# Optimization experiments

Hardware: AMD Instinct MI355X
Metric: run time of the kernel (lower is better)

The kernel has to match this reference:

```python
import jax, jax.numpy as jnp
import numpy as np

N = 50000
E = 600000
D = 128


def gcn_conv(x, row, col, w, W, b):
    """PyG GCNConv: add self-loops (weight 1), symmetric deg^-1/2 normalization,
    linear transform, edge-weighted scatter-add aggregation, then bias."""
    n = x.shape[0]
    loop = jnp.arange(n)
    r = jnp.concatenate([row, loop])            # source nodes, [E+N]
    c = jnp.concatenate([col, loop])            # target nodes, [E+N]
    ww = jnp.concatenate([w, jnp.ones((n,), x.dtype)])
    deg = jax.ops.segment_sum(ww, c, num_segments=n)          # weighted in-degree
    dinv = jnp.where(deg > 0, jax.lax.rsqrt(deg), jnp.zeros_like(deg))
    norm = dinv[r] * ww * dinv[c]               # [E+N]
    xl = x @ W                                  # [n, D_out]
    msg = norm[:, None] * xl[r]                 # gather + scale, [E+N, D_out]
    out = jax.ops.segment_sum(msg, c, num_segments=n)
    return out + b


def setup_inputs() -> dict:
    key = jax.random.key(0)
    ks = jax.random.split(key, 12)
    x = jax.random.normal(ks[0], (N, D), dtype=jnp.float32)
    edge_index = jax.random.randint(ks[1], (2, E), 0, N, dtype=jnp.int64)
    edge_weights = jax.random.uniform(ks[2], (E,), dtype=jnp.float32)
    s = 1.0 / np.sqrt(D)
    W1 = jax.random.uniform(ks[3], (D, D), jnp.float32, -s, s)
    b1 = jnp.zeros((D,), jnp.float32)
    W2 = jax.random.uniform(ks[4], (D, D), jnp.float32, -s, s)
    b2 = jnp.zeros((D,), jnp.float32)
    W3 = jax.random.uniform(ks[5], (D, D), jnp.float32, -s, s)
    b3 = jnp.zeros((D,), jnp.float32)
    prelu_w = jnp.array(0.25, jnp.float32)
    return {"x": x, "edge_index": edge_index, "edge_weights": edge_weights,
            "W1": W1, "b1": b1, "W2": W2, "b2": b2, "W3": W3, "b3": b3,
            "prelu_w": prelu_w}


def reference(x, edge_index, edge_weights, W1, b1, W2, b2, W3, b3, prelu_w):
    row, col = edge_index[0], edge_index[1]
    # layer 1: GCNConv -> (dropout: eval, identity) -> ELU
    h = gcn_conv(x, row, col, edge_weights, W1, b1)
    h = jax.nn.elu(h)
    # layer 2: GCNConv -> GELU (torch default = exact erf)
    h = gcn_conv(h, row, col, edge_weights, W2, b2)
    h = jax.nn.gelu(h, approximate=False)
    # layer 3: GCNConv -> PReLU (learnable scalar slope)
    h = gcn_conv(h, row, col, edge_weights, W3, b3)
    h = jnp.where(h >= 0, h, prelu_w * h)
    return h
```

## Files before the change

### kernel.cpp

```cpp
#include <hip/hip_runtime.h>
#include <hip/hip_fp16.h>
#include <math.h>
#include <string.h>

constexpr int D = 128;

struct __align__(16) H8 { __half2 h[4]; };
struct __align__(8)  H4 { __half2 a, b; };

typedef _Float16 half8  __attribute__((ext_vector_type(8)));
typedef float   floatx4 __attribute__((ext_vector_type(4)));
typedef int     i32x4   __attribute__((ext_vector_type(4)));

template <typename T>
__device__ __forceinline__ T ld_nt(const T* p) {
  if constexpr (sizeof(T) == 16) {
    i32x4 v = __builtin_nontemporal_load((const i32x4*)p);
    T r; memcpy(&r, &v, 16); return r;
  } else {
    int v = __builtin_nontemporal_load((const int*)p);
    T r; memcpy(&r, &v, 4); return r;
  }
}
__device__ __forceinline__ void st_nt16(void* p, float4 v) {
  i32x4 t; memcpy(&t, &v, 16);
  __builtin_nontemporal_store(t, (i32x4*)p);
}


__device__ __forceinline__ int detect64(const int* __restrict__ ei) {
  int z = 0;
#pragma unroll
  for (int i = 0; i < 8; ++i) z |= ei[2 * i + 1];
  return (z == 0) ? 1 : 0;
}

__device__ __forceinline__ void load_edge(const int* __restrict__ ei, int e, int nE,
                                          int m64, int n, int& r, int& c) {
  if (m64) { r = ei[2 * (size_t)e]; c = ei[2 * ((size_t)nE + e)]; }
  else     { r = ei[(size_t)e];     c = ei[(size_t)nE + e]; }
  r = min(max(r, 0), n - 1);
  c = min(max(c, 0), n - 1);
}

__global__ void k_init(const float* __restrict__ W1, const float* __restrict__ W2,
                       const float* __restrict__ W3, __half* __restrict__ Wt,
                       int* __restrict__ cnt, int n) {
  __shared__ float s[128][129];
  int tid = threadIdx.x;
  if (blockIdx.x >= 3) {
    int i = (blockIdx.x - 3) * 256 + tid;
    if (i < n) cnt[i] = 0;
    return;
  }
  const float* W = blockIdx.x == 0 ? W1 : (blockIdx.x == 1 ? W2 : W3);
  __half* o = Wt + (size_t)blockIdx.x * D * D;
#pragma unroll
  for (int i = 0; i < 16; ++i) {
    int flat = i * 1024 + tid * 4;
    int k = flat >> 7;
    int nn = flat & 127;
    float4 v = *(const float4*)(W + (size_t)k * D + nn);
    s[k][nn] = v.x; s[k][nn + 1] = v.y; s[k][nn + 2] = v.z; s[k][nn + 3] = v.w;
  }
  __syncthreads();
#pragma unroll
  for (int i = 0; i < 8; ++i) {
    int flat = i * 256 + tid;
    int nn = flat >> 4;
    int k0 = (flat & 15) * 8;
    H8 hv;
#pragma unroll
    for (int t = 0; t < 4; ++t)
      hv.h[t] = __floats2half2_rn(s[k0 + 2 * t][nn], s[k0 + 2 * t + 1][nn]);
    *(H8*)(o + (size_t)nn * D + k0) = hv;
  }
}

__global__ void k_pos(const int* __restrict__ ei, int* __restrict__ cnt,
                      unsigned int* __restrict__ rcp, int* __restrict__ pos,
                      int nE, int n) {
  int e = blockIdx.x * blockDim.x + threadIdx.x;
  if (e >= nE) return;
  int m64 = detect64(ei);
  int r, c;
  load_edge(ei, e, nE, m64, n, r, c);
  rcp[e] = ((unsigned int)r << 16) | (unsigned int)c;
  pos[e] = atomicAdd(&cnt[c], 1);
}

__global__ void k_scan1(const int* __restrict__ cnt, int* __restrict__ offs,
                        int* __restrict__ bsum, int n) {
  __shared__ int s[256];
  int t = threadIdx.x;
  int i = blockIdx.x * 256 + t;
  int v = (i < n) ? cnt[i] : 0;
  s[t] = v;
  __syncthreads();
  for (int off = 1; off < 256; off <<= 1) {
    int x = 0;
    if (t >= off) x = s[t - off];
    __syncthreads();
    if (t >= off) s[t] += x;
    __syncthreads();
  }
  if (i < n) offs[i] = s[t] - v;
  if (t == 255) bsum[blockIdx.x] = s[255];
}

__global__ void k_scan2(const int* __restrict__ bsum, int* __restrict__ boff, int nb) {
  __shared__ int s[256];
  int t = threadIdx.x;
  int v = (t < nb) ? bsum[t] : 0;
  s[t] = v;
  __syncthreads();
  for (int off = 1; off < 256; off <<= 1) {
    int x = 0;
    if (t >= off) x = s[t - off];
    __syncthreads();
    if (t >= off) s[t] += x;
    __syncthreads();
  }
  if (t < nb) boff[t] = s[t] - v;
}

__global__ void k_scan3(int* __restrict__ offs, const int* __restrict__ boff, int n, int nE) {
  int i = blockIdx.x * 256 + threadIdx.x;
  if (i < n) offs[i] += boff[blockIdx.x];
  if (i == 0) offs[n] = nE;
}

__global__ void k_fill(const unsigned int* __restrict__ rcp, const int* __restrict__ pos,
                       const float* __restrict__ w, const int* __restrict__ offs,
                       int2* __restrict__ ecf, int nE) {
  int e = blockIdx.x * blockDim.x + threadIdx.x;
  if (e >= nE) return;
  unsigned int p = rcp[e];
  int idx = offs[p & 0xffffu] + pos[e];
  ecf[idx] = make_int2((int)(p >> 16), __float_as_int(w[e]));
}

__global__ void k_degdinv(const int2* __restrict__ ecf, const int* __restrict__ offs,
                          float* __restrict__ dinv, int n) {
  int i = blockIdx.x * blockDim.x + threadIdx.x;
  if (i >= n) return;
  float s = 1.0f;
  int e1 = offs[i + 1];
  for (int e = offs[i]; e < e1; ++e) s += __int_as_float(ecf[e].y);
  dinv[i] = rsqrtf(s);
}

__global__ void k_coef(const int2* __restrict__ ecf, const float* __restrict__ dinv,
                       unsigned int* __restrict__ ecf2, int nE) {
  int e = blockIdx.x * blockDim.x + threadIdx.x;
  if (e >= nE) return;
  int2 p = ecf[e];
  float c = dinv[p.x] * __int_as_float(p.y);
  ecf2[e] = ((unsigned int)p.x << 16) |
            (unsigned int)__half_as_ushort(__float2half_rn(c));
}

template <int ACT>
__device__ __forceinline__ float act_f(float x) {
  if (ACT == 1) return x > 0.f ? x : expm1f(x);
  if (ACT == 2) return 0.5f * x * (1.0f + erff(x * 0.70710678118654752440f));
  return x;
}

template <int ACT, typename AT>
__global__ __launch_bounds__(256) void k_gemm(const AT* __restrict__ A,
                                              const __half* __restrict__ Wt,
                                              __half* __restrict__ Y, int n) {
  const int wave = threadIdx.x >> 6;
  const int lane = threadIdx.x & 63;
  const int np = lane & 15;
  const int quad = lane >> 4;
  const int node = blockIdx.x * 64 + wave * 16 + np;
  const int nc = min(node, n - 1);

  half8 b[4];
#pragma unroll
  for (int s = 0; s < 4; ++s) {
    if constexpr (sizeof(AT) == 4) {
      const float* ap = (const float*)A + (size_t)nc * D + s * 32 + quad * 8;
      float4 v0 = ld_nt((const float4*)ap);
      float4 v1 = ld_nt((const float4*)(ap + 4));
      b[s][0] = (_Float16)act_f<ACT>(v0.x); b[s][1] = (_Float16)act_f<ACT>(v0.y);
      b[s][2] = (_Float16)act_f<ACT>(v0.z); b[s][3] = (_Float16)act_f<ACT>(v0.w);
      b[s][4] = (_Float16)act_f<ACT>(v1.x); b[s][5] = (_Float16)act_f<ACT>(v1.y);
      b[s][6] = (_Float16)act_f<ACT>(v1.z); b[s][7] = (_Float16)act_f<ACT>(v1.w);
    } else {
      half8 raw = *(const half8*)((const __half*)A + ((size_t)s * n + nc) * 32 + quad * 8);
#pragma unroll
      for (int t = 0; t < 8; ++t)
        b[s][t] = (_Float16)act_f<ACT>((float)raw[t]);
    }
  }

  floatx4 acc[8];
#pragma unroll
  for (int mt = 0; mt < 8; ++mt) acc[mt] = (floatx4){0.f, 0.f, 0.f, 0.f};

#pragma unroll
  for (int mt = 0; mt < 8; ++mt) {
#pragma unroll
    for (int s = 0; s < 4; ++s) {
      half8 a = *(const half8*)(Wt + (size_t)(mt * 16 + np) * D + s * 32 + quad * 8);
      acc[mt] = __builtin_amdgcn_mfma_f32_16x16x32_f16(a, b[s], acc[mt], 0, 0, 0);
    }
  }

  if (node < n) {
#pragma unroll
    for (int mt = 0; mt < 8; ++mt) {
      H4 hv;
      hv.a = __floats2half2_rn(acc[mt][0], acc[mt][1]);
      hv.b = __floats2half2_rn(acc[mt][2], acc[mt][3]);
      int f0 = mt * 16 + quad * 4;
      *(H4*)(Y + ((size_t)(f0 >> 5) * n + node) * 32 + (f0 & 31)) = hv;
    }
  }
}

__device__ __forceinline__ void fmacc8(float* acc, float c, const H8& y) {
  float2 f;
  f = __half22float2(y.h[0]); acc[0] += c * f.x; acc[1] += c * f.y;
  f = __half22float2(y.h[1]); acc[2] += c * f.x; acc[3] += c * f.y;
  f = __half22float2(y.h[2]); acc[4] += c * f.x; acc[5] += c * f.y;
  f = __half22float2(y.h[3]); acc[6] += c * f.x; acc[7] += c * f.y;
}

__device__ __forceinline__ float cdecode(unsigned int u) {
  return __half2float(__ushort_as_half((unsigned short)(u & 0xffffu)));
}

template <int PRELU, typename OutT>
__global__ __launch_bounds__(256) void k_agg(const __half* __restrict__ Y,
                                             const int* __restrict__ offs,
                                             const unsigned int* __restrict__ ecf2,
                                             const float* __restrict__ dinv,
                                             const float* __restrict__ bias,
                                             const float* __restrict__ pw,
                                             OutT* __restrict__ OUT, int n) {
  const int chunk = blockIdx.x & 3;
  const int t = threadIdx.x;
  const int node = (blockIdx.x >> 2) * 32 + (t >> 3);
  const int sub = (t >> 2) & 1;
  const int j = t & 3;
  if (node >= n) return;
  const __half* Yc = Y + (size_t)chunk * n * 32;
  float dc = dinv[node];
  float acc[8] = {0.f, 0.f, 0.f, 0.f, 0.f, 0.f, 0.f, 0.f};
  if (sub == 0) {
    H8 ys = *(const H8*)(Yc + (size_t)node * 32 + j * 8);
    fmacc8(acc, dc, ys);
  }
  int e0 = offs[node], e1 = offs[node + 1];
  int e = e0 + sub;
  for (; e + 6 < e1; e += 8) {
    unsigned int u0 = ld_nt(&ecf2[e]),     u1 = ld_nt(&ecf2[e + 2]);
    unsigned int u2 = ld_nt(&ecf2[e + 4]), u3 = ld_nt(&ecf2[e + 6]);
    H8 y0 = *(const H8*)(Yc + (size_t)(u0 >> 16) * 32 + j * 8);
    H8 y1 = *(const H8*)(Yc + (size_t)(u1 >> 16) * 32 + j * 8);
    H8 y2 = *(const H8*)(Yc + (size_t)(u2 >> 16) * 32 + j * 8);
    H8 y3 = *(const H8*)(Yc + (size_t)(u3 >> 16) * 32 + j * 8);
    fmacc8(acc, cdecode(u0), y0);
    fmacc8(acc, cdecode(u1), y1);
    fmacc8(acc, cdecode(u2), y2);
    fmacc8(acc, cdecode(u3), y3);
  }
  for (; e + 2 < e1; e += 4) {
    unsigned int u0 = ld_nt(&ecf2[e]), u1 = ld_nt(&ecf2[e + 2]);
    H8 y0 = *(const H8*)(Yc + (size_t)(u0 >> 16) * 32 + j * 8);
    H8 y1 = *(const H8*)(Yc + (size_t)(u1 >> 16) * 32 + j * 8);
    fmacc8(acc, cdecode(u0), y0);
    fmacc8(acc, cdecode(u1), y1);
  }
  for (; e < e1; e += 2) {
    unsigned int u = ld_nt(&ecf2[e]);
    H8 y = *(const H8*)(Yc + (size_t)(u >> 16) * 32 + j * 8);
    fmacc8(acc, cdecode(u), y);
  }
#pragma unroll
  for (int i = 0; i < 8; ++i) acc[i] += __shfl_xor(acc[i], 4, 64);
  float4 b4 = *(const float4*)(bias + chunk * 32 + j * 8 + sub * 4);
  float o[4];
  o[0] = dc * acc[sub * 4 + 0] + b4.x;
  o[1] = dc * acc[sub * 4 + 1] + b4.y;
  o[2] = dc * acc[sub * 4 + 2] + b4.z;
  o[3] = dc * acc[sub * 4 + 3] + b4.w;
  if (PRELU) {
    float wv = *pw;
#pragma unroll
    for (int i = 0; i < 4; ++i) o[i] = o[i] >= 0.f ? o[i] : wv * o[i];
  }
  if constexpr (sizeof(OutT) == 4) {
    st_nt16((float*)OUT + (size_t)node * D + chunk * 32 + j * 8 + sub * 4,
            make_float4(o[0], o[1], o[2], o[3]));
  } else {
    H4 hv;
    hv.a = __floats2half2_rn(o[0], o[1]);
    hv.b = __floats2half2_rn(o[2], o[3]);
    *(H4*)((__half*)OUT + ((size_t)chunk * n + node) * 32 + j * 8 + sub * 4) = hv;
  }
}

extern "C" void kernel_launch(void* const* d_in, const int* in_sizes, int n_in,
                              void* d_out, int out_size, void* d_ws, size_t ws_size,
                              hipStream_t stream) {
  const float* x  = (const float*)d_in[0];
  const int*   ei = (const int*)d_in[1];
  const float* w  = (const float*)d_in[2];
  const float* W1 = (const float*)d_in[3];
  const float* b1 = (const float*)d_in[4];
  const float* W2 = (const float*)d_in[5];
  const float* b2 = (const float*)d_in[6];
  const float* W3 = (const float*)d_in[7];
  const float* b3 = (const float*)d_in[8];
  const float* pw = (const float*)d_in[9];
  const int N = in_sizes[0] / D;
  const int E = in_sizes[2];
  float* out = (float*)d_out;

  char* wsb = (char*)d_ws;
  size_t off = 0;
  auto alloc = [&](size_t bytes) {
    void* p = wsb + off;
    off = (off + bytes + 255) & ~(size_t)255;
    return p;
  };
  float*        dinv = (float*)alloc((size_t)N * 4);
  int*          cnt  = (int*)alloc((size_t)N * 4);
  int*          offs = (int*)alloc((size_t)(N + 1) * 4);
  int*          bsum = (int*)alloc(256 * 4);
  int*          boff = (int*)alloc(256 * 4);
  int2*         ecf  = (int2*)alloc((size_t)E * 8);
  unsigned int* ecf2 = (unsigned int*)alloc((size_t)E * 4);
  __half*       Wt   = (__half*)alloc((size_t)3 * D * D * 2);
  __half*       Y    = (__half*)alloc((size_t)N * D * 2);
  __half*       h    = (__half*)alloc((size_t)N * D * 2);
  unsigned int* rcp  = (unsigned int*)Y;
  int*          pos  = (int*)((char*)Y + (size_t)E * 4);

  const int nb = (N + 255) / 256;
  const int eb = (E + 255) / 256;

  hipLaunchKernelGGL(k_init,    dim3(3 + nb), dim3(256), 0, stream, W1, W2, W3, Wt, cnt, N);
  hipLaunchKernelGGL(k_pos,     dim3(eb), dim3(256), 0, stream, ei, cnt, rcp, pos, E, N);
  hipLaunchKernelGGL(k_scan1,   dim3(nb), dim3(256), 0, stream, cnt, offs, bsum, N);
  hipLaunchKernelGGL(k_scan2,   dim3(1),  dim3(256), 0, stream, bsum, boff, nb);
  hipLaunchKernelGGL(k_scan3,   dim3(nb), dim3(256), 0, stream, offs, boff, N, E);
  hipLaunchKernelGGL(k_fill,    dim3(eb), dim3(256), 0, stream, rcp, pos, w, offs, ecf, E);
  hipLaunchKernelGGL(k_degdinv, dim3(nb), dim3(256), 0, stream, ecf, offs, dinv, N);
  hipLaunchKernelGGL(k_coef,    dim3(eb), dim3(256), 0, stream, ecf, dinv, ecf2, E);

  const int gb = (N + 63) / 64;
  const int ab = 4 * ((N + 31) / 32);

  hipLaunchKernelGGL((k_gemm<0, float>),  dim3(gb), dim3(256), 0, stream, x, Wt,             Y, N);
  hipLaunchKernelGGL((k_agg<0, __half>),  dim3(ab), dim3(256), 0, stream, Y, offs, ecf2, dinv, b1, pw, h, N);
  hipLaunchKernelGGL((k_gemm<1, __half>), dim3(gb), dim3(256), 0, stream, h, Wt + D * D,     Y, N);
  hipLaunchKernelGGL((k_agg<0, __half>),  dim3(ab), dim3(256), 0, stream, Y, offs, ecf2, dinv, b2, pw, h, N);
  hipLaunchKernelGGL((k_gemm<2, __half>), dim3(gb), dim3(256), 0, stream, h, Wt + 2 * D * D, Y, N);
  hipLaunchKernelGGL((k_agg<1, float>),   dim3(ab), dim3(256), 0, stream, Y, offs, ecf2, dinv, b3, pw, out, N);
}
```

Measured before the change: 328.7 us.

## Fold source dinv into GEMM output, drop coef pass, single-block scan, wider agg split

The source-side normalisation dinv[r] moves into the GEMM epilogue, so Z = dinv*xW and the edge coefficient becomes just the raw weight stored as fp16. This removes the k_coef kernel and the 8-byte ecf intermediate. The three-kernel scan becomes one 1024-thread single-block scan built on wave shuffles. The aggregation kernel now uses 16 threads per node-chunk (4 edge lanes instead of 2) with an extra shuffle reduction, and drops nontemporal loads on the edge list. The trade-off is that the serial single-block scan may be slower, and storing edge weights in fp16 before the degree sum costs some precision.

New measurement: 344.2 us. 1.05x slower.

```diff
diff --git a/kernel.cpp b/kernel.cpp
--- a/kernel.cpp
+++ b/kernel.cpp
@@ -14,17 +14,12 @@
 
 template <typename T>
 __device__ __forceinline__ T ld_nt(const T* p) {
-  if constexpr (sizeof(T) == 16) {
-    i32x4 v = __builtin_nontemporal_load((const i32x4*)p);
-    T r; memcpy(&r, &v, 16); return r;
-  } else {
-    int v = __builtin_nontemporal_load((const int*)p);
-    T r; memcpy(&r, &v, 4); return r;
-  }
-}
-__device__ __forceinline__ void st_nt16(void* p, float4 v) {
-  i32x4 t; memcpy(&t, &v, 16);
-  __builtin_nontemporal_store(t, (i32x4*)p);
+  i32x4 v = __builtin_nontemporal_load((const i32x4*)p);
+  T r; memcpy(&r, &v, 16); return r;
+}
+__device__ __forceinline__ void st_nt8(void* p, float2 v) {
+  long long t; memcpy(&t, &v, 8);
+  __builtin_nontemporal_store(t, (long long*)p);
 }
 
 
@@ -89,75 +84,63 @@
   pos[e] = atomicAdd(&cnt[c], 1);
 }
 
-__global__ void k_scan1(const int* __restrict__ cnt, int* __restrict__ offs,
-                        int* __restrict__ bsum, int n) {
-  __shared__ int s[256];
-  int t = threadIdx.x;
-  int i = blockIdx.x * 256 + t;
-  int v = (i < n) ? cnt[i] : 0;
-  s[t] = v;
-  __syncthreads();
-  for (int off = 1; off < 256; off <<= 1) {
-    int x = 0;
-    if (t >= off) x = s[t - off];
+__global__ __launch_bounds__(1024) void k_scan(const int* __restrict__ cnt,
+                                               int* __restrict__ offs, int n, int nE) {
+  __shared__ int wsx[16];
+  __shared__ int tot;
+  const int t = threadIdx.x;
+  const int lane = t & 63, wid = t >> 6;
+  int carry = 0;
+  for (int base = 0; base < n; base += 1024) {
+    int i = base + t;
+    int v = (i < n) ? cnt[i] : 0;
+    int s = v;
+#pragma unroll
+    for (int d = 1; d < 64; d <<= 1) {
+      int x = __shfl_up(s, d, 64);
+      if (lane >= d) s += x;
+    }
+    if (lane == 63) wsx[wid] = s;
     __syncthreads();
-    if (t >= off) s[t] += x;
+    if (t < 16) {
+      int ws = wsx[t];
+      int ss = ws;
+#pragma unroll
+      for (int d = 1; d < 16; d <<= 1) {
+        int x = __shfl_up(ss, d, 16);
+        if (t >= d) ss += x;
+      }
+      wsx[t] = ss - ws;
+      if (t == 15) tot = ss;
+    }
     __syncthreads();
-  }
-  if (i < n) offs[i] = s[t] - v;
-  if (t == 255) bsum[blockIdx.x] = s[255];
-}
-
-__global__ void k_scan2(const int* __restrict__ bsum, int* __restrict__ boff, int nb) {
-  __shared__ int s[256];
-  int t = threadIdx.x;
-  int v = (t < nb) ? bsum[t] : 0;
-  s[t] = v;
-  __syncthreads();
-  for (int off = 1; off < 256; off <<= 1) {
-    int x = 0;
-    if (t >= off) x = s[t - off];
+    if (i < n) offs[i] = carry + wsx[wid] + (s - v);
+    carry += tot;
     __syncthreads();
-    if (t >= off) s[t] += x;
-    __syncthreads();
-  }
-  if (t < nb) boff[t] = s[t] - v;
-}
-
-__global__ void k_scan3(int* __restrict__ offs, const int* __restrict__ boff, int n, int nE) {
-  int i = blockIdx.x * 256 + threadIdx.x;
-  if (i < n) offs[i] += boff[blockIdx.x];
-  if (i == 0) offs[n] = nE;
+  }
+  if (t == 0) offs[n] = nE;
 }
 
 __global__ void k_fill(const unsigned int* __restrict__ rcp, const int* __restrict__ pos,
                        const float* __restrict__ w, const int* __restrict__ offs,
-                       int2* __restrict__ ecf, int nE) {
+                       unsigned int* __restrict__ ecf2, int nE) {
   int e = blockIdx.x * blockDim.x + threadIdx.x;
   if (e >= nE) return;
   unsigned int p = rcp[e];
   int idx = offs[p & 0xffffu] + pos[e];
-  ecf[idx] = make_int2((int)(p >> 16), __float_as_int(w[e]));
-}
-
-__global__ void k_degdinv(const int2* __restrict__ ecf, const int* __restrict__ offs,
+  ecf2[idx] = (p & 0xffff0000u) |
+              (unsigned int)__half_as_ushort(__float2half_rn(w[e]));
+}
+
+__global__ void k_degdinv(const unsigned int* __restrict__ ecf2, const int* __restrict__ offs,
                           float* __restrict__ dinv, int n) {
   int i = blockIdx.x * blockDim.x + threadIdx.x;
   if (i >= n) return;
   float s = 1.0f;
   int e1 = offs[i + 1];
-  for (int e = offs[i]; e < e1; ++e) s += __int_as_float(ecf[e].y);
+  for (int e = offs[i]; e < e1; ++e)
+    s += __half2float(__ushort_as_half((unsigned short)(ecf2[e] & 0xffffu)));
   dinv[i] = rsqrtf(s);
-}
-
-__global__ void k_coef(const int2* __restrict__ ecf, const float* __restrict__ dinv,
-                       unsigned int* __restrict__ ecf2, int nE) {
-  int e = blockIdx.x * blockDim.x + threadIdx.x;
-  if (e >= nE) return;
-  int2 p = ecf[e];
-  float c = dinv[p.x] * __int_as_float(p.y);
-  ecf2[e] = ((unsigned int)p.x << 16) |
-            (unsigned int)__half_as_ushort(__float2half_rn(c));
 }
 
 template <int ACT>
@@ -170,7 +153,8 @@
 template <int ACT, typename AT>
 __global__ __launch_bounds__(256) void k_gemm(const AT* __restrict__ A,
                                               const __half* __restrict__ Wt,
-                                              __half* __restrict__ Y, int n) {
+                                              const float* __restrict__ dinv,
+                                              __half* __restrict__ Z, int n) {
   const int wave = threadIdx.x >> 6;
   const int lane = threadIdx.x & 63;
   const int np = lane & 15;
@@ -211,13 +195,14 @@
   }
 
   if (node < n) {
+    float dv = dinv[node];
 #pragma unroll
     for (int mt = 0; mt < 8; ++mt) {
       H4 hv;
-      hv.a = __floats2half2_rn(acc[mt][0], acc[mt][1]);
-      hv.b = __floats2half2_rn(acc[mt][2], acc[mt][3]);
+      hv.a = __floats2half2_rn(dv * acc[mt][0], dv * acc[mt][1]);
+      hv.b = __floats2half2_rn(dv * acc[mt][2], dv * acc[mt][3]);
       int f0 = mt * 16 + quad * 4;
-      *(H4*)(Y + ((size_t)(f0 >> 5) * n + node) * 32 + (f0 & 31)) = hv;
+      *(H4*)(Z + ((size_t)(f0 >> 5) * n + node) * 32 + (f0 & 31)) = hv;
     }
   }
 }
@@ -235,7 +220,7 @@
 }
 
 template <int PRELU, typename OutT>
-__global__ __launch_bounds__(256) void k_agg(const __half* __restrict__ Y,
+__global__ __launch_bounds__(256) void k_agg(const __half* __restrict__ Z,
                                              const int* __restrict__ offs,
                                              const unsigned int* __restrict__ ecf2,
                                              const float* __restrict__ dinv,
@@ -244,64 +229,62 @@
                                              OutT* __restrict__ OUT, int n) {
   const int chunk = blockIdx.x & 3;
   const int t = threadIdx.x;
-  const int node = (blockIdx.x >> 2) * 32 + (t >> 3);
-  const int sub = (t >> 2) & 1;
+  const int node = (blockIdx.x >> 2) * 16 + (t >> 4);
+  const int sub = (t >> 2) & 3;
   const int j = t & 3;
   if (node >= n) return;
-  const __half* Yc = Y + (size_t)chunk * n * 32;
-  float dc = dinv[node];
+  const __half* Zc = Z + (size_t)chunk * n * 32;
   float acc[8] = {0.f, 0.f, 0.f, 0.f, 0.f, 0.f, 0.f, 0.f};
   if (sub == 0) {
-    H8 ys = *(const H8*)(Yc + (size_t)node * 32 + j * 8);
-    fmacc8(acc, dc, ys);
+    H8 zs = *(const H8*)(Zc + (size_t)node * 32 + j * 8);
+    fmacc8(acc, 1.0f, zs);
   }
   int e0 = offs[node], e1 = offs[node + 1];
   int e = e0 + sub;
-  for (; e + 6 < e1; e += 8) {
-    unsigned int u0 = ld_nt(&ecf2[e]),     u1 = ld_nt(&ecf2[e + 2]);
-    unsigned int u2 = ld_nt(&ecf2[e + 4]), u3 = ld_nt(&ecf2[e + 6]);
-    H8 y0 = *(const H8*)(Yc + (size_t)(u0 >> 16) * 32 + j * 8);
-    H8 y1 = *(const H8*)(Yc + (size_t)(u1 >> 16) * 32 + j * 8);
-    H8 y2 = *(const H8*)(Yc + (size_t)(u2 >> 16) * 32 + j * 8);
-    H8 y3 = *(const H8*)(Yc + (size_t)(u3 >> 16) * 32 + j * 8);
-    fmacc8(acc, cdecode(u0), y0);
-    fmacc8(acc, cdecode(u1), y1);
-    fmacc8(acc, cdecode(u2), y2);
-    fmacc8(acc, cdecode(u3), y3);
-  }
-  for (; e + 2 < e1; e += 4) {
-    unsigned int u0 = ld_nt(&ecf2[e]), u1 = ld_nt(&ecf2[e + 2]);
-    H8 y0 = *(const H8*)(Yc + (size_t)(u0 >> 16) * 32 + j * 8);
-    H8 y1 = *(const H8*)(Yc + (size_t)(u1 >> 16) * 32 + j * 8);
-    fmacc8(acc, cdecode(u0), y0);
-    fmacc8(acc, cdecode(u1), y1);
-  }
-  for (; e < e1; e += 2) {
-    unsigned int u = ld_nt(&ecf2[e]);
-    H8 y = *(const H8*)(Yc + (size_t)(u >> 16) * 32 + j * 8);
-    fmacc8(acc, cdecode(u), y);
-  }
-#pragma unroll
-  for (int i = 0; i < 8; ++i) acc[i] += __shfl_xor(acc[i], 4, 64);
-  float4 b4 = *(const float4*)(bias + chunk * 32 + j * 8 + sub * 4);
-  float o[4];
-  o[0] = dc * acc[sub * 4 + 0] + b4.x;
-  o[1] = dc * acc[sub * 4 + 1] + b4.y;
-  o[2] = dc * acc[sub * 4 + 2] + b4.z;
-  o[3] = dc * acc[sub * 4 + 3] + b4.w;
+  for (; e + 12 < e1; e += 16) {
+    unsigned int u0 = ecf2[e],     u1 = ecf2[e + 4];
+    unsigned int u2 = ecf2[e + 8], u3 = ecf2[e + 12];
+    H8 z0 = *(const H8*)(Zc + (size_t)(u0 >> 16) * 32 + j * 8);
+    H8 z1 = *(const H8*)(Zc + (size_t)(u1 >> 16) * 32 + j * 8);
+    H8 z2 = *(const H8*)(Zc + (size_t)(u2 >> 16) * 32 + j * 8);
+    H8 z3 = *(const H8*)(Zc + (size_t)(u3 >> 16) * 32 + j * 8);
+    fmacc8(acc, cdecode(u0), z0);
+    fmacc8(acc, cdecode(u1), z1);
+    fmacc8(acc, cdecode(u2), z2);
+    fmacc8(acc, cdecode(u3), z3);
+  }
+  for (; e + 4 < e1; e += 8) {
+    unsigned int u0 = ecf2[e], u1 = ecf2[e + 4];
+    H8 z0 = *(const H8*)(Zc + (size_t)(u0 >> 16) * 32 + j * 8);
+    H8 z1 = *(const H8*)(Zc + (size_t)(u1 >> 16) * 32 + j * 8);
+    fmacc8(acc, cdecode(u0), z0);
+    fmacc8(acc, cdecode(u1), z1);
+  }
+  for (; e < e1; e += 4) {
+    unsigned int u = ecf2[e];
+    H8 z = *(const H8*)(Zc + (size_t)(u >> 16) * 32 + j * 8);
+    fmacc8(acc, cdecode(u), z);
+  }
+#pragma unroll
+  for (int i = 0; i < 8; ++i) {
+    acc[i] += __shfl_xor(acc[i], 4, 64);
+    acc[i] += __shfl_xor(acc[i], 8, 64);
+  }
+  float dc = dinv[node];
+  const float* bp = bias + chunk * 32 + j * 8 + sub * 2;
+  float o0 = dc * acc[sub * 2 + 0] + bp[0];
+  float o1 = dc * acc[sub * 2 + 1] + bp[1];
   if (PRELU) {
     float wv = *pw;
-#pragma unroll
-    for (int i = 0; i < 4; ++i) o[i] = o[i] >= 0.f ? o[i] : wv * o[i];
+    o0 = o0 >= 0.f ? o0 : wv * o0;
+    o1 = o1 >= 0.f ? o1 : wv * o1;
   }
   if constexpr (sizeof(OutT) == 4) {
-    st_nt16((float*)OUT + (size_t)node * D + chunk * 32 + j * 8 + sub * 4,
-            make_float4(o[0], o[1], o[2], o[3]));
+    st_nt8((float*)OUT + (size_t)node * D + chunk * 32 + j * 8 + sub * 2,
+           make_float2(o0, o1));
   } else {
-    H4 hv;
-    hv.a = __floats2half2_rn(o[0], o[1]);
-    hv.b = __floats2half2_rn(o[2], o[3]);
-    *(H4*)((__half*)OUT + ((size_t)chunk * n + node) * 32 + j * 8 + sub * 4) = hv;
+    *(__half2*)((__half*)OUT + ((size_t)chunk * n + node) * 32 + j * 8 + sub * 2) =
+        __floats2half2_rn(o0, o1);
   }
 }
 
@@ -332,35 +315,29 @@
   float*        dinv = (float*)alloc((size_t)N * 4);
   int*          cnt  = (int*)alloc((size_t)N * 4);
   int*          offs = (int*)alloc((size_t)(N + 1) * 4);
-  int*          bsum = (int*)alloc(256 * 4);
-  int*          boff = (int*)alloc(256 * 4);
-  int2*         ecf  = (int2*)alloc((size_t)E * 8);
   unsigned int* ecf2 = (unsigned int*)alloc((size_t)E * 4);
   __half*       Wt   = (__half*)alloc((size_t)3 * D * D * 2);
-  __half*       Y    = (__half*)alloc((size_t)N * D * 2);
+  __half*       Z    = (__half*)alloc((size_t)N * D * 2);
   __half*       h    = (__half*)alloc((size_t)N * D * 2);
-  unsigned int* rcp  = (unsigned int*)Y;
-  int*          pos  = (int*)((char*)Y + (size_t)E * 4);
+  unsigned int* rcp  = (unsigned int*)Z;
+  int*          pos  = (int*)((char*)Z + (size_t)E * 4);
 
   const int nb = (N + 255) / 256;
   const int eb = (E + 255) / 256;
 
   hipLaunchKernelGGL(k_init,    dim3(3 + nb), dim3(256), 0, stream, W1, W2, W3, Wt, cnt, N);
   hipLaunchKernelGGL(k_pos,     dim3(eb), dim3(256), 0, stream, ei, cnt, rcp, pos, E, N);
-  hipLaunchKernelGGL(k_scan1,   dim3(nb), dim3(256), 0, stream, cnt, offs, bsum, N);
-  hipLaunchKernelGGL(k_scan2,   dim3(1),  dim3(256), 0, stream, bsum, boff, nb);
-  hipLaunchKernelGGL(k_scan3,   dim3(nb), dim3(256), 0, stream, offs, boff, N, E);
-  hipLaunchKernelGGL(k_fill,    dim3(eb), dim3(256), 0, stream, rcp, pos, w, offs, ecf, E);
-  hipLaunchKernelGGL(k_degdinv, dim3(nb), dim3(256), 0, stream, ecf, offs, dinv, N);
-  hipLaunchKernelGGL(k_coef,    dim3(eb), dim3(256), 0, stream, ecf, dinv, ecf2, E);
+  hipLaunchKernelGGL(k_scan,    dim3(1),  dim3(1024), 0, stream, cnt, offs, N, E);
+  hipLaunchKernelGGL(k_fill,    dim3(eb), dim3(256), 0, stream, rcp, pos, w, offs, ecf2, E);
+  hipLaunchKernelGGL(k_degdinv, dim3(nb), dim3(256), 0, stream, ecf2, offs, dinv, N);
 
   const int gb = (N + 63) / 64;
-  const int ab = 4 * ((N + 31) / 32);
-
-  hipLaunchKernelGGL((k_gemm<0, float>),  dim3(gb), dim3(256), 0, stream, x, Wt,             Y, N);
-  hipLaunchKernelGGL((k_agg<0, __half>),  dim3(ab), dim3(256), 0, stream, Y, offs, ecf2, dinv, b1, pw, h, N);
-  hipLaunchKernelGGL((k_gemm<1, __half>), dim3(gb), dim3(256), 0, stream, h, Wt + D * D,     Y, N);
-  hipLaunchKernelGGL((k_agg<0, __half>),  dim3(ab), dim3(256), 0, stream, Y, offs, ecf2, dinv, b2, pw, h, N);
-  hipLaunchKernelGGL((k_gemm<2, __half>), dim3(gb), dim3(256), 0, stream, h, Wt + 2 * D * D, Y, N);
-  hipLaunchKernelGGL((k_agg<1, float>),   dim3(ab), dim3(256), 0, stream, Y, offs, ecf2, dinv, b3, pw, out, N);
-}
+  const int ab = 4 * ((N + 15) / 16);
+
+  hipLaunchKernelGGL((k_gemm<0, float>),  dim3(gb), dim3(256), 0, stream, x, Wt,             dinv, Z, N);
+  hipLaunchKernelGGL((k_agg<0, __half>),  dim3(ab), dim3(256), 0, stream, Z, offs, ecf2, dinv, b1, pw, h, N);
+  hipLaunchKernelGGL((k_gemm<1, __half>), dim3(gb), dim3(256), 0, stream, h, Wt + D * D,     dinv, Z, N);
+  hipLaunchKernelGGL((k_agg<0, __half>),  dim3(ab), dim3(256), 0, stream, Z, offs, ecf2, dinv, b2, pw, h, N);
+  hipLaunchKernelGGL((k_gemm<2, __half>), dim3(gb), dim3(256), 0, stream, h, Wt + 2 * D * D, dinv, Z, N);
+  hipLaunchKernelGGL((k_agg<1, float>),   dim3(ab), dim3(256), 0, stream, Z, offs, ecf2, dinv, b3, pw, out, N);
+}
```
